# Kernel optimization log

Measured on AMD Instinct MI355X. Metric: run time of the kernel, lower is better.

The kernel has to match this reference:

```python
import jax, jax.numpy as jnp
import numpy as np

N, D_IN, D, E, B = 30000, 512, 512, 300000, 4096
N_RES, N_DNN = 2, 2
EPS = 1e-5


def _ln(x, g, b):
    mu = jnp.mean(x, axis=-1, keepdims=True)
    var = jnp.mean((x - mu) ** 2, axis=-1, keepdims=True)
    return (x - mu) * jax.lax.rsqrt(var + EPS) * g + b


def setup_inputs() -> dict:
    key = jax.random.key(0)
    ks = jax.random.split(key, 16)
    s = 1.0 / np.sqrt(D)
    inp = {
        "node_feat": jax.random.normal(ks[0], (N, D_IN), jnp.float32),
        "edge_hop0": jax.random.randint(ks[1], (2, E), 0, N, jnp.int32),
        "edge_hop1": jax.random.randint(ks[2], (2, E), 0, N, jnp.int32),
        "target_idx": jax.random.randint(ks[3], (B,), 0, N, jnp.int32),
        # node transform
        "Wt": jax.random.normal(ks[4], (D_IN, D), jnp.float32) / np.sqrt(D_IN),
        "bt": jnp.zeros((D,), jnp.float32),
        # GATConv (shared across both hops, one relation)
        "Wf": jax.random.normal(ks[5], (D, D), jnp.float32) * s,
        "bf": jnp.zeros((D,), jnp.float32),
        "w_att": jax.random.normal(ks[6], (2 * D,), jnp.float32) * s,
        "b_att": jnp.zeros((), jnp.float32),
        "gat_bias": jnp.zeros((D,), jnp.float32),
        # Res_DNN
        "Wp": jax.random.normal(ks[7], (D, D), jnp.float32) * s,
        "bp": jnp.zeros((D,), jnp.float32),
        "dnn_W": jax.random.normal(ks[8], (N_RES, N_DNN, D, D), jnp.float32) * s,
        "dnn_b": jnp.zeros((N_RES, N_DNN, D), jnp.float32),
        "dnn_g": jnp.ones((N_RES, N_DNN, D), jnp.float32),
        "dnn_beta": jnp.zeros((N_RES, N_DNN, D), jnp.float32),
        "res_g": jnp.ones((N_RES, D), jnp.float32),
        "res_beta": jnp.zeros((N_RES, D), jnp.float32),
        "Wc": jax.random.normal(ks[9], (D, 1), jnp.float32) * s,
        "bc": jnp.zeros((1,), jnp.float32),
    }
    return inp


def _gat(feat, edges, Wf, bf, w_att, b_att, gat_bias):
    # dst and src are the same node set / same features here
    h = feat @ Wf + bf                      # [N, D]
    di, si = edges[0], edges[1]             # [E], [E]
    # att(concat(dst_h, src_h)) == dst_h @ w[:D] + src_h @ w[D:] + b
    sd = h @ w_att[:D]                      # [N]
    ss = h @ w_att[D:]                      # [N]
    e = jnp.tanh(sd[di] + ss[si] + b_att)   # [E]
    # sparse softmax per destination row
    m = jax.ops.segment_max(e, di, num_segments=N)
    a = jnp.exp(e - m[di])
    denom = jax.ops.segment_sum(a, di, num_segments=N)
    alpha = a / denom[di]                   # [E]
    # sparse-mm aggregation
    out = jax.ops.segment_sum(alpha[:, None] * h[si], di, num_segments=N)
    return out + gat_bias


def reference(node_feat, edge_hop0, edge_hop1, target_idx, Wt, bt, Wf, bf,
              w_att, b_att, gat_bias, Wp, bp, dnn_W, dnn_b, dnn_g, dnn_beta,
              res_g, res_beta, Wc, bc):
    # node-type feature transform (dropout is identity at inference)
    feat = node_feat @ Wt + bt              # [N, D]
    # hops processed from last to first: hop1 then hop0
    for edges in (edge_hop1, edge_hop0):
        g = _gat(feat, edges, Wf, bf, w_att, b_att, gat_bias)
        feat = (feat + g) * 0.5             # mean of stacked [orig, gat_out]
    h = feat[target_idx]                    # [B, D]
    # Res_DNN head
    h = h @ Wp + bp
    for r in range(N_RES):
        sc = h
        for i in range(N_DNN):
            h = _ln(jnp.tanh(h @ dnn_W[r, i] + dnn_b[r, i]), dnn_g[r, i], dnn_beta[r, i])
        h = _ln(jnp.tanh(sc + h), res_g[r], res_beta[r])
    logits = h @ Wc + bc                    # [B, 1]
    return jax.nn.sigmoid(logits)
```

## Files before the change

### kernel.cpp

```cpp
#include <hip/hip_runtime.h>

#define D 512
typedef unsigned short ushort_t;
typedef __attribute__((ext_vector_type(8))) short bf16x8;
typedef __attribute__((ext_vector_type(4))) float f32x4;

static __device__ __forceinline__ ushort_t f2bf(float f) {
  unsigned u = __float_as_uint(f);
  u += 0x7fffu + ((u >> 16) & 1u);
  return (ushort_t)(u >> 16);
}
static __device__ __forceinline__ float bf2f(ushort_t h) {
  return __uint_as_float(((unsigned)h) << 16);
}

static __device__ __forceinline__ void gld_lds16(const void* g, void* lds) {
  __builtin_amdgcn_global_load_lds(
      (const __attribute__((address_space(1))) unsigned int*)g,
      (__attribute__((address_space(3))) unsigned int*)lds, 16, 0, 0);
}

__global__ __launch_bounds__(256) void pack_weight(
    const float* __restrict__ W, ushort_t* __restrict__ out, int K, int N, int nmat) {
  int i = blockIdx.x * 256 + threadIdx.x;
  const int per = K * N;
  if (i >= per * nmat) return;
  const int mat = i / per;
  const int r = i - mat * per;
  const int k = r / N, n = r - k * N;
  const int nt = n >> 4, col = n & 15, kt = k >> 5, kg = (k >> 3) & 3, j = k & 7;
  out[(size_t)mat * per + (((size_t)nt * (K >> 5) + kt) << 9) + ((kg << 4) + col) * 8 + j] =
      f2bf(W[(size_t)mat * per + r]);
}

__global__ __launch_bounds__(256) void conv_bf16_pad(
    const float* __restrict__ in, ushort_t* __restrict__ out, int M, int Mp, int K) {
  const size_t i4 = ((size_t)blockIdx.x * 256 + threadIdx.x) * 4;
  if (i4 >= (size_t)Mp * K) return;
  const int row = (int)(i4 / K);
  ushort4 o;
  if (row < M) {
    const float4 v = *reinterpret_cast<const float4*>(&in[i4]);
    o.x = f2bf(v.x); o.y = f2bf(v.y); o.z = f2bf(v.z); o.w = f2bf(v.w);
  } else {
    o.x = o.y = o.z = o.w = 0;
  }
  *reinterpret_cast<ushort4*>(&out[i4]) = o;
}

__global__ __launch_bounds__(256) void gemm_mfma(
    const ushort_t* __restrict__ A, const ushort_t* __restrict__ Bp,
    const float* __restrict__ bias, ushort_t* __restrict__ C16, int N, int K) {
  __shared__ __align__(16) ushort_t As[2][8 * 512];
  __shared__ __align__(16) ushort_t Bs[2][8 * 512];
  const int nwg = gridDim.x;
  const int q = nwg >> 3, rm = nwg & 7;
  const int xcd = blockIdx.x & 7, kk = blockIdx.x >> 3;
  const int lin = (xcd < rm ? xcd * (q + 1) : rm * (q + 1) + (xcd - rm) * q) + kk;
  const int m0 = (lin >> 2) * 128;
  const int n0 = (lin & 3) * 128;
  const int tid = threadIdx.x;
  const int lane = tid & 63;
  const int wid = tid >> 6;
  const int wm = wid >> 1, wn = wid & 1;
  const int arow = lane & 15;
  const int akoff = (lane >> 4) * 8;
  const int kt32 = K >> 5;
  f32x4 acc[4][4] = {};

  auto stage = [&](int kt, int b) {
    const int k0 = kt * 32;
    gld_lds16(&A[(size_t)(m0 + (wid * 2 + 0) * 16 + arow) * K + k0 + akoff],
              &As[b][(wid * 2 + 0) * 512]);
    gld_lds16(&A[(size_t)(m0 + (wid * 2 + 1) * 16 + arow) * K + k0 + akoff],
              &As[b][(wid * 2 + 1) * 512]);
    gld_lds16(&Bp[(((size_t)(n0 / 16 + wid * 2 + 0) * kt32 + kt) << 9) + lane * 8],
              &Bs[b][(wid * 2 + 0) * 512]);
    gld_lds16(&Bp[(((size_t)(n0 / 16 + wid * 2 + 1) * kt32 + kt) << 9) + lane * 8],
              &Bs[b][(wid * 2 + 1) * 512]);
  };

  stage(0, 0);
  __syncthreads();
  int cur = 0;
  for (int t = 0; t < kt32; ++t) {
    if (t + 1 < kt32) stage(t + 1, cur ^ 1);
    bf16x8 af[4], bfr[4];
#pragma unroll
    for (int mi = 0; mi < 4; ++mi)
      af[mi] = *reinterpret_cast<const bf16x8*>(&As[cur][(wm * 4 + mi) * 512 + lane * 8]);
#pragma unroll
    for (int ni = 0; ni < 4; ++ni)
      bfr[ni] = *reinterpret_cast<const bf16x8*>(&Bs[cur][(wn * 4 + ni) * 512 + lane * 8]);
#pragma unroll
    for (int mi = 0; mi < 4; ++mi)
#pragma unroll
      for (int ni = 0; ni < 4; ++ni)
        acc[mi][ni] = __builtin_amdgcn_mfma_f32_16x16x32_bf16(af[mi], bfr[ni], acc[mi][ni], 0, 0, 0);
    __syncthreads();
    cur ^= 1;
  }
#pragma unroll
  for (int mi = 0; mi < 4; ++mi) {
    const int row = m0 + wm * 64 + mi * 16 + ((lane >> 4) << 2);
#pragma unroll
    for (int ni = 0; ni < 4; ++ni) {
      const int col = n0 + wn * 64 + ni * 16 + (lane & 15);
      const float bv = bias[col];
#pragma unroll
      for (int r = 0; r < 4; ++r)
        C16[(size_t)(row + r) * N + col] = f2bf(acc[mi][ni][r] + bv);
    }
  }
}

__global__ __launch_bounds__(256) void rowdot2_w(
    const ushort_t* __restrict__ hb, const float* __restrict__ w_att,
    float* __restrict__ sd, float* __restrict__ ss, int Nn) {
  const int r = blockIdx.x * 4 + (threadIdx.x >> 6);
  const int lane = threadIdx.x & 63;
  if (r >= Nn) return;
  const bf16x8 hv = *reinterpret_cast<const bf16x8*>(&hb[(size_t)r * D + lane * 8]);
  float d0 = 0.f, d1 = 0.f;
#pragma unroll
  for (int q = 0; q < 8; ++q) {
    const float v = bf2f((ushort_t)hv[q]);
    d0 += v * w_att[lane * 8 + q];
    d1 += v * w_att[D + lane * 8 + q];
  }
#pragma unroll
  for (int off = 32; off > 0; off >>= 1) {
    d0 += __shfl_xor(d0, off);
    d1 += __shfl_xor(d1, off);
  }
  if (lane == 0) { sd[r] = d0; ss[r] = d1; }
}

__global__ void count_deg2(const int* __restrict__ e1, const int* __restrict__ e0,
                           int* __restrict__ deg, int Nn, int E) {
  const int e = blockIdx.x * blockDim.x + threadIdx.x;
  if (e < E) {
    atomicAdd(&deg[e1[e]], 1);
    atomicAdd(&deg[Nn + e0[e]], 1);
  }
}

__global__ __launch_bounds__(256) void scan_block(
    const int* __restrict__ deg, int* __restrict__ incl, int* __restrict__ bsum, int n) {
  __shared__ int buf[256];
  const int t = threadIdx.x;
  const int i = blockIdx.x * 256 + t;
  const int v = (i < n) ? deg[i] : 0;
  buf[t] = v;
  __syncthreads();
  for (int off = 1; off < 256; off <<= 1) {
    const int y = (t >= off) ? buf[t - off] : 0;
    __syncthreads();
    buf[t] += y;
    __syncthreads();
  }
  if (i < n) incl[i] = buf[t];
  if (t == 255) bsum[blockIdx.x] = buf[255];
}

__global__ __launch_bounds__(256) void scan_sums(
    int* __restrict__ bsum, int nb, int* __restrict__ row_total) {
  __shared__ int buf[256];
  const int t = threadIdx.x;
  const int v = (t < nb) ? bsum[t] : 0;
  buf[t] = v;
  __syncthreads();
  for (int off = 1; off < 256; off <<= 1) {
    const int y = (t >= off) ? buf[t - off] : 0;
    __syncthreads();
    buf[t] += y;
    __syncthreads();
  }
  if (t < nb) bsum[t] = buf[t] - v;
  if (t == 0) *row_total = buf[255];
}

__global__ __launch_bounds__(256) void scan_finalize(
    const int* __restrict__ incl, const int* __restrict__ deg,
    const int* __restrict__ bsum, int* __restrict__ row_start,
    int* __restrict__ cursor, int n) {
  const int i = blockIdx.x * 256 + threadIdx.x;
  if (i >= n) return;
  const int v = incl[i] - deg[i] + bsum[i >> 8];
  row_start[i] = v;
  cursor[i] = v;
}

__global__ void fill_csr2(const int* __restrict__ e1, const int* __restrict__ e0,
                          int* __restrict__ cursor, int* __restrict__ csr_s,
                          int Nn, int E) {
  const int e = blockIdx.x * blockDim.x + threadIdx.x;
  if (e >= E) return;
  const int d1 = e1[e];
  csr_s[atomicAdd(&cursor[d1], 1)] = e1[E + e];
  const int d0 = e0[e];
  csr_s[atomicAdd(&cursor[Nn + d0], 1)] = e0[E + e];
}

__global__ __launch_bounds__(256) void gat_aggregate_w(
    ushort_t* __restrict__ featb, const ushort_t* __restrict__ hb,
    const float* __restrict__ sd, const float* __restrict__ ss,
    float* __restrict__ edge_e, const float* __restrict__ b_att_p,
    const float* __restrict__ gat_bias, const int* __restrict__ row_start,
    const int* __restrict__ csr_src, int Nn) {
  const int dst = blockIdx.x * 4 + (threadIdx.x >> 6);
  const int lane = threadIdx.x & 63;
  if (dst >= Nn) return;
  const int beg = row_start[dst];
  const int end = row_start[dst + 1];
  const int deg = end - beg;
  const float sdd = sd[dst];
  const float ba = b_att_p[0];
  const size_t o = (size_t)dst * D + lane * 8;
  bf16x8 fv = *reinterpret_cast<const bf16x8*>(&featb[o]);
  float acc[8] = {};
  if (deg <= 64) {
    const int j0 = beg + lane;
    const bool valid = j0 < end;
    const int slane = valid ? csr_src[j0] : 0;
    const float e = valid ? tanhf(sdd + ss[slane] + ba) : -1e30f;
    float m = e;
#pragma unroll
    for (int off = 32; off > 0; off >>= 1) m = fmaxf(m, __shfl_xor(m, off));
    const float a = valid ? expf(e - m) : 0.f;
    float s = a;
#pragma unroll
    for (int off = 32; off > 0; off >>= 1) s += __shfl_xor(s, off);
    const float w = a * ((s > 0.f) ? 1.f / s : 0.f);
    int k = 0;
    for (; k + 3 < deg; k += 4) {
      const float w0 = __shfl(w, k), w1 = __shfl(w, k + 1);
      const float w2 = __shfl(w, k + 2), w3 = __shfl(w, k + 3);
      const int s0 = __shfl(slane, k), s1 = __shfl(slane, k + 1);
      const int s2 = __shfl(slane, k + 2), s3 = __shfl(slane, k + 3);
      const bf16x8 h0 = *reinterpret_cast<const bf16x8*>(&hb[(size_t)s0 * D + lane * 8]);
      const bf16x8 h1 = *reinterpret_cast<const bf16x8*>(&hb[(size_t)s1 * D + lane * 8]);
      const bf16x8 h2 = *reinterpret_cast<const bf16x8*>(&hb[(size_t)s2 * D + lane * 8]);
      const bf16x8 h3 = *reinterpret_cast<const bf16x8*>(&hb[(size_t)s3 * D + lane * 8]);
#pragma unroll
      for (int qq = 0; qq < 8; ++qq)
        acc[qq] += w0 * bf2f((ushort_t)h0[qq]) + w1 * bf2f((ushort_t)h1[qq]) +
                   w2 * bf2f((ushort_t)h2[qq]) + w3 * bf2f((ushort_t)h3[qq]);
    }
    for (; k < deg; ++k) {
      const float wk = __shfl(w, k);
      const int sk = __shfl(slane, k);
      const bf16x8 h0 = *reinterpret_cast<const bf16x8*>(&hb[(size_t)sk * D + lane * 8]);
#pragma unroll
      for (int qq = 0; qq < 8; ++qq) acc[qq] += wk * bf2f((ushort_t)h0[qq]);
    }
  } else {
    float m = -1e30f;
    for (int j = beg + lane; j < end; j += 64) {
      const float e = tanhf(sdd + ss[csr_src[j]] + ba);
      edge_e[j] = e;
      m = fmaxf(m, e);
    }
#pragma unroll
    for (int off = 32; off > 0; off >>= 1) m = fmaxf(m, __shfl_xor(m, off));
    asm volatile("s_waitcnt vmcnt(0)" ::: "memory");
    float s = 0.f;
    for (int j = beg + lane; j < end; j += 64) {
      const float a2 = expf(edge_e[j] - m);
      edge_e[j] = a2;
      s += a2;
    }
#pragma unroll
    for (int off = 32; off > 0; off >>= 1) s += __shfl_xor(s, off);
    asm volatile("s_waitcnt vmcnt(0)" ::: "memory");
    const float inv = (s > 0.f) ? 1.f / s : 0.f;
    for (int j = beg; j < end; ++j) {
      const float w = edge_e[j] * inv;
      const int sidx = csr_src[j];
      const bf16x8 hv = *reinterpret_cast<const bf16x8*>(&hb[(size_t)sidx * D + lane * 8]);
#pragma unroll
      for (int qq = 0; qq < 8; ++qq) acc[qq] += w * bf2f((ushort_t)hv[qq]);
    }
  }
#pragma unroll
  for (int q = 0; q < 8; ++q) {
    const float f = (bf2f((ushort_t)fv[q]) + acc[q] + gat_bias[lane * 8 + q]) * 0.5f;
    fv[q] = (short)f2bf(f);
  }
  *reinterpret_cast<bf16x8*>(&featb[o]) = fv;
}

__global__ __launch_bounds__(1024, 4) void head_fused(
    const ushort_t* __restrict__ featb, const int* __restrict__ tidx,
    const ushort_t* __restrict__ pWp, const float* __restrict__ bp,
    const ushort_t* __restrict__ pDW, const float* __restrict__ dnn_b,
    const float* __restrict__ dnn_g, const float* __restrict__ dnn_be,
    const float* __restrict__ res_g, const float* __restrict__ res_be,
    const float* __restrict__ Wc, const float* __restrict__ bc,
    float* __restrict__ out) {
  __shared__ __align__(16) ushort_t A_lds[16 * 512];
  __shared__ float lsum[16][16], lsq[16][16], meanv[16], rsv[16];
  const int tid = threadIdx.x;
  const int lane = tid & 63;
  const int wave = tid >> 6;
  const int nt0 = wave * 2;
  const int c15 = lane & 15;
  const int rgrp = lane >> 4;

  {
    const int row = tid >> 6, col8 = tid & 63;
    const int g = tidx[blockIdx.x * 16 + row];
    const bf16x8 v = *reinterpret_cast<const bf16x8*>(&featb[(size_t)g * D + col8 * 8]);
    *reinterpret_cast<bf16x8*>(&A_lds[row * 512 + (col8 ^ (row & 7)) * 8]) = v;
  }
  __syncthreads();

  auto do_gemm = [&](const ushort_t* __restrict__ W, f32x4& a0, f32x4& a1) {
    a0 = f32x4{0.f, 0.f, 0.f, 0.f};
    a1 = f32x4{0.f, 0.f, 0.f, 0.f};
    bf16x8 c0 = *reinterpret_cast<const bf16x8*>(
        &W[(((size_t)nt0 * 16 + 0) << 9) + lane * 8]);
    bf16x8 c1 = *reinterpret_cast<const bf16x8*>(
        &W[(((size_t)(nt0 + 1) * 16 + 0) << 9) + lane * 8]);
#pragma unroll
    for (int kt = 0; kt < 16; ++kt) {
      bf16x8 n0 = c0, n1 = c1;
      if (kt < 15) {
        n0 = *reinterpret_cast<const bf16x8*>(
            &W[(((size_t)nt0 * 16 + kt + 1) << 9) + lane * 8]);
        n1 = *reinterpret_cast<const bf16x8*>(
            &W[(((size_t)(nt0 + 1) * 16 + kt + 1) << 9) + lane * 8]);
      }
      const int col8 = kt * 4 + rgrp;
      const bf16x8 af = *reinterpret_cast<const bf16x8*>(
          &A_lds[c15 * 512 + (col8 ^ (c15 & 7)) * 8]);
      a0 = __builtin_amdgcn_mfma_f32_16x16x32_bf16(af, c0, a0, 0, 0, 0);
      a1 = __builtin_amdgcn_mfma_f32_16x16x32_bf16(af, c1, a1, 0, 0, 0);
      c0 = n0;
      c1 = n1;
    }
  };

  auto block_ln = [&](f32x4& v0, f32x4& v1, const float* __restrict__ g,
                      const float* __restrict__ be) {
    float psum[4], psq[4];
#pragma unroll
    for (int r = 0; r < 4; ++r) {
      psum[r] = v0[r] + v1[r];
      psq[r] = v0[r] * v0[r] + v1[r] * v1[r];
    }
#pragma unroll
    for (int off = 8; off > 0; off >>= 1)
#pragma unroll
      for (int r = 0; r < 4; ++r) {
        psum[r] += __shfl_xor(psum[r], off);
        psq[r] += __shfl_xor(psq[r], off);
      }
    if (c15 == 0) {
#pragma unroll
      for (int r = 0; r < 4; ++r) {
        lsum[wave][rgrp * 4 + r] = psum[r];
        lsq[wave][rgrp * 4 + r] = psq[r];
      }
    }
    __syncthreads();
    if (tid < 16) {
      float s = 0.f, qq = 0.f;
#pragma unroll
      for (int w = 0; w < 16; ++w) { s += lsum[w][tid]; qq += lsq[w][tid]; }
      const float mean = s * (1.f / 512.f);
      const float var = qq * (1.f / 512.f) - mean * mean;
      meanv[tid] = mean;
      rsv[tid] = rsqrtf(var + 1e-5f);
    }
    __syncthreads();
    const int col0 = nt0 * 16 + c15;
    const int col1 = (nt0 + 1) * 16 + c15;
    const float g0 = g[col0], b0 = be[col0];
    const float g1 = g[col1], b1 = be[col1];
#pragma unroll
    for (int r = 0; r < 4; ++r) {
      const int row = rgrp * 4 + r;
      v0[r] = (v0[r] - meanv[row]) * rsv[row] * g0 + b0;
      v1[r] = (v1[r] - meanv[row]) * rsv[row] * g1 + b1;
    }
  };

  auto store_A = [&](const f32x4& v0, const f32x4& v1) {
    const int col0 = nt0 * 16 + c15;
    const int col1 = (nt0 + 1) * 16 + c15;
#pragma unroll
    for (int r = 0; r < 4; ++r) {
      const int row = rgrp * 4 + r;
      A_lds[row * 512 + (((col0 >> 3) ^ (row & 7)) << 3) + (col0 & 7)] = f2bf(v0[r]);
      A_lds[row * 512 + (((col1 >> 3) ^ (row & 7)) << 3) + (col1 & 7)] = f2bf(v1[r]);
    }
  };

  f32x4 sc0, sc1, acc0, acc1, ln0, ln1;

  do_gemm(pWp, acc0, acc1);
  {
    const float bv0 = bp[nt0 * 16 + c15];
    const float bv1 = bp[(nt0 + 1) * 16 + c15];
#pragma unroll
    for (int r = 0; r < 4; ++r) { sc0[r] = acc0[r] + bv0; sc1[r] = acc1[r] + bv1; }
  }
  __syncthreads();
  store_A(sc0, sc1);
  __syncthreads();

  for (int rb = 0; rb < 2; ++rb) {
    {
      const int st = rb * 2;
      do_gemm(pDW + (size_t)st * D * D, acc0, acc1);
      const float bv0 = dnn_b[st * D + nt0 * 16 + c15];
      const float bv1 = dnn_b[st * D + (nt0 + 1) * 16 + c15];
#pragma unroll
      for (int r = 0; r < 4; ++r) {
        acc0[r] = tanhf(acc0[r] + bv0);
        acc1[r] = tanhf(acc1[r] + bv1);
      }
      block_ln(acc0, acc1, dnn_g + st * D, dnn_be + st * D);
      store_A(acc0, acc1);
      __syncthreads();
    }
    {
      const int st = rb * 2 + 1;
      do_gemm(pDW + (size_t)st * D * D, ln0, ln1);
      const float bv0 = dnn_b[st * D + nt0 * 16 + c15];
      const float bv1 = dnn_b[st * D + (nt0 + 1) * 16 + c15];
#pragma unroll
      for (int r = 0; r < 4; ++r) {
        ln0[r] = tanhf(ln0[r] + bv0);
        ln1[r] = tanhf(ln1[r] + bv1);
      }
      block_ln(ln0, ln1, dnn_g + st * D, dnn_be + st * D);
    }
#pragma unroll
    for (int r = 0; r < 4; ++r) {
      acc0[r] = tanhf(sc0[r] + ln0[r]);
      acc1[r] = tanhf(sc1[r] + ln1[r]);
    }
    block_ln(acc0, acc1, res_g + rb * D, res_be + rb * D);
    sc0 = acc0;
    sc1 = acc1;
    if (rb == 0) {
      store_A(sc0, sc1);
      __syncthreads();
    }
  }

  float pr[4];
  {
    const float w0 = Wc[nt0 * 16 + c15];
    const float w1 = Wc[(nt0 + 1) * 16 + c15];
#pragma unroll
    for (int r = 0; r < 4; ++r) pr[r] = sc0[r] * w0 + sc1[r] * w1;
  }
#pragma unroll
  for (int off = 8; off > 0; off >>= 1)
#pragma unroll
    for (int r = 0; r < 4; ++r) pr[r] += __shfl_xor(pr[r], off);
  __syncthreads();
  if (c15 == 0) {
#pragma unroll
    for (int r = 0; r < 4; ++r) lsum[wave][rgrp * 4 + r] = pr[r];
  }
  __syncthreads();
  if (tid < 16) {
    float s = 0.f;
#pragma unroll
    for (int w = 0; w < 16; ++w) s += lsum[w][tid];
    out[blockIdx.x * 16 + tid] = 1.f / (1.f + expf(-(s + bc[0])));
  }
}

extern "C" void kernel_launch(void* const* d_in, const int* in_sizes, int n_in,
                              void* d_out, int out_size, void* d_ws, size_t ws_size,
                              hipStream_t stream) {
  (void)n_in; (void)out_size; (void)ws_size;
  const float* node_feat = (const float*)d_in[0];
  const int* edge0 = (const int*)d_in[1];
  const int* edge1 = (const int*)d_in[2];
  const int* tidx = (const int*)d_in[3];
  const float* Wt = (const float*)d_in[4];
  const float* bt = (const float*)d_in[5];
  const float* Wf = (const float*)d_in[6];
  const float* bfp = (const float*)d_in[7];
  const float* w_att = (const float*)d_in[8];
  const float* b_att = (const float*)d_in[9];
  const float* gat_bias = (const float*)d_in[10];
  const float* Wp = (const float*)d_in[11];
  const float* bp = (const float*)d_in[12];
  const float* dnn_W = (const float*)d_in[13];
  const float* dnn_b = (const float*)d_in[14];
  const float* dnn_g = (const float*)d_in[15];
  const float* dnn_be = (const float*)d_in[16];
  const float* res_g = (const float*)d_in[17];
  const float* res_be = (const float*)d_in[18];
  const float* Wc = (const float*)d_in[19];
  const float* bc = (const float*)d_in[20];
  float* out = (float*)d_out;

  const int Nn = in_sizes[0] / D;
  const int E = in_sizes[1] / 2;
  const int B = in_sizes[3];
  const int K_IN = in_sizes[4] / D;
  const int Mp = (Nn + 127) / 128 * 128;
  const int N2 = 2 * Nn;

  char* p = (char*)d_ws;
  auto alloc = [&](size_t bytes) -> char* {
    char* r = p;
    p += (bytes + 255) & ~(size_t)255;
    return r;
  };
  ushort_t* featb = (ushort_t*)alloc((size_t)Mp * D * 2);
  ushort_t* hb = (ushort_t*)alloc((size_t)Mp * D * 2);
  float* sd = (float*)alloc((size_t)Nn * 4);
  float* ss = (float*)alloc((size_t)Nn * 4);
  int* deg = (int*)alloc((size_t)N2 * 4);
  int* incl = (int*)alloc((size_t)N2 * 4);
  int* bsum = (int*)alloc(256 * 4);
  int* cursor = (int*)alloc((size_t)N2 * 4);
  int* row_start = (int*)alloc((size_t)(N2 + 1) * 4);
  int* csr_s = (int*)alloc((size_t)2 * E * 4);
  float* edge_e = (float*)alloc((size_t)2 * E * 4);
  ushort_t* pWt = (ushort_t*)alloc((size_t)K_IN * D * 2);
  ushort_t* pWf = (ushort_t*)alloc((size_t)D * D * 2);
  ushort_t* pWp = (ushort_t*)alloc((size_t)D * D * 2);
  ushort_t* pDWall = (ushort_t*)alloc((size_t)4 * D * D * 2);

  dim3 blk(256);
  const int nb2 = (N2 + 255) / 256;
  const int nw4 = (Nn + 3) / 4;

  {
    pack_weight<<<(K_IN * D + 255) / 256, blk, 0, stream>>>(Wt, pWt, K_IN, D, 1);
    pack_weight<<<(D * D + 255) / 256, blk, 0, stream>>>(Wf, pWf, D, D, 1);
    pack_weight<<<(D * D + 255) / 256, blk, 0, stream>>>(Wp, pWp, D, D, 1);
    pack_weight<<<(4 * D * D + 255) / 256, blk, 0, stream>>>(dnn_W, pDWall, D, D, 4);
    conv_bf16_pad<<<((size_t)Mp * K_IN / 4 + 255) / 256, blk, 0, stream>>>(
        node_feat, hb , Nn, Mp, K_IN);
  }

  hipMemsetAsync(deg, 0, (size_t)N2 * 4, stream);
  count_deg2<<<(E + 255) / 256, blk, 0, stream>>>(edge1, edge0, deg, Nn, E);
  scan_block<<<nb2, blk, 0, stream>>>(deg, incl, bsum, N2);
  scan_sums<<<1, blk, 0, stream>>>(bsum, nb2, &row_start[N2]);
  scan_finalize<<<nb2, blk, 0, stream>>>(incl, deg, bsum, row_start, cursor, N2);
  fill_csr2<<<(E + 255) / 256, blk, 0, stream>>>(edge1, edge0, cursor, csr_s, Nn, E);

  gemm_mfma<<<dim3(4 * (Mp / 128)), blk, 0, stream>>>(hb, pWt, bt, featb, D, K_IN);

  for (int hp = 0; hp < 2; ++hp) {
    gemm_mfma<<<dim3(4 * (Mp / 128)), blk, 0, stream>>>(featb, pWf, bfp, hb, D, D);
    rowdot2_w<<<nw4, blk, 0, stream>>>(hb, w_att, sd, ss, Nn);
    gat_aggregate_w<<<nw4, blk, 0, stream>>>(featb, hb, sd, ss, edge_e, b_att,
                                             gat_bias, row_start + hp * Nn, csr_s, Nn);
  }

  head_fused<<<B / 16, dim3(1024), 0, stream>>>(
      featb, tidx, pWp, bp, pDWall, dnn_b, dnn_g, dnn_be, res_g, res_be,
      Wc, bc, out);
}
```

Measured before the change: 355.4 us.

## Replace CSR build with fixed-width per-node buckets and edge-scan fallback

Drops the degree count, three-kernel prefix scan and CSR fill. In their place one atomic pass writes each edge's source into a fixed 64-slot bucket per destination node. Nodes with more than 64 incoming edges fall back to scanning the whole edge list, which is slow but correct. The aggregation inner loop is also unrolled from 4 to 8 gathers to keep more loads in flight. This trades several small launches and passes for a larger bucket buffer, and relies on degrees staying at or below 64, which holds for uniform random edges (mean degree about 10).

Measured after the change: 340.7 us. 1.04x faster.

```diff
diff --git a/kernel.cpp b/kernel.cpp
--- a/kernel.cpp
+++ b/kernel.cpp
@@ -136,93 +136,37 @@
   if (lane == 0) { sd[r] = d0; ss[r] = d1; }
 }
 
-__global__ void count_deg2(const int* __restrict__ e1, const int* __restrict__ e0,
-                           int* __restrict__ deg, int Nn, int E) {
-  const int e = blockIdx.x * blockDim.x + threadIdx.x;
-  if (e < E) {
-    atomicAdd(&deg[e1[e]], 1);
-    atomicAdd(&deg[Nn + e0[e]], 1);
-  }
-}
-
-__global__ __launch_bounds__(256) void scan_block(
-    const int* __restrict__ deg, int* __restrict__ incl, int* __restrict__ bsum, int n) {
-  __shared__ int buf[256];
-  const int t = threadIdx.x;
-  const int i = blockIdx.x * 256 + t;
-  const int v = (i < n) ? deg[i] : 0;
-  buf[t] = v;
-  __syncthreads();
-  for (int off = 1; off < 256; off <<= 1) {
-    const int y = (t >= off) ? buf[t - off] : 0;
-    __syncthreads();
-    buf[t] += y;
-    __syncthreads();
-  }
-  if (i < n) incl[i] = buf[t];
-  if (t == 255) bsum[blockIdx.x] = buf[255];
-}
-
-__global__ __launch_bounds__(256) void scan_sums(
-    int* __restrict__ bsum, int nb, int* __restrict__ row_total) {
-  __shared__ int buf[256];
-  const int t = threadIdx.x;
-  const int v = (t < nb) ? bsum[t] : 0;
-  buf[t] = v;
-  __syncthreads();
-  for (int off = 1; off < 256; off <<= 1) {
-    const int y = (t >= off) ? buf[t - off] : 0;
-    __syncthreads();
-    buf[t] += y;
-    __syncthreads();
-  }
-  if (t < nb) bsum[t] = buf[t] - v;
-  if (t == 0) *row_total = buf[255];
-}
-
-__global__ __launch_bounds__(256) void scan_finalize(
-    const int* __restrict__ incl, const int* __restrict__ deg,
-    const int* __restrict__ bsum, int* __restrict__ row_start,
-    int* __restrict__ cursor, int n) {
-  const int i = blockIdx.x * 256 + threadIdx.x;
-  if (i >= n) return;
-  const int v = incl[i] - deg[i] + bsum[i >> 8];
-  row_start[i] = v;
-  cursor[i] = v;
-}
-
-__global__ void fill_csr2(const int* __restrict__ e1, const int* __restrict__ e0,
-                          int* __restrict__ cursor, int* __restrict__ csr_s,
-                          int Nn, int E) {
+__global__ void fill_bucket(const int* __restrict__ e1, const int* __restrict__ e0,
+                            int* __restrict__ cnt, int* __restrict__ bucket,
+                            int Nn, int E) {
   const int e = blockIdx.x * blockDim.x + threadIdx.x;
   if (e >= E) return;
   const int d1 = e1[e];
-  csr_s[atomicAdd(&cursor[d1], 1)] = e1[E + e];
+  const int p1 = atomicAdd(&cnt[d1], 1);
+  if (p1 < 64) bucket[(size_t)d1 * 64 + p1] = e1[E + e];
   const int d0 = e0[e];
-  csr_s[atomicAdd(&cursor[Nn + d0], 1)] = e0[E + e];
+  const int p0 = atomicAdd(&cnt[Nn + d0], 1);
+  if (p0 < 64) bucket[((size_t)(Nn + d0)) * 64 + p0] = e0[E + e];
 }
 
 __global__ __launch_bounds__(256) void gat_aggregate_w(
     ushort_t* __restrict__ featb, const ushort_t* __restrict__ hb,
     const float* __restrict__ sd, const float* __restrict__ ss,
-    float* __restrict__ edge_e, const float* __restrict__ b_att_p,
-    const float* __restrict__ gat_bias, const int* __restrict__ row_start,
-    const int* __restrict__ csr_src, int Nn) {
+    const int* __restrict__ di, const int* __restrict__ si,
+    const float* __restrict__ b_att_p, const float* __restrict__ gat_bias,
+    const int* __restrict__ cnt, const int* __restrict__ bucket, int Nn, int E) {
   const int dst = blockIdx.x * 4 + (threadIdx.x >> 6);
   const int lane = threadIdx.x & 63;
   if (dst >= Nn) return;
-  const int beg = row_start[dst];
-  const int end = row_start[dst + 1];
-  const int deg = end - beg;
+  const int deg = cnt[dst];
   const float sdd = sd[dst];
   const float ba = b_att_p[0];
   const size_t o = (size_t)dst * D + lane * 8;
   bf16x8 fv = *reinterpret_cast<const bf16x8*>(&featb[o]);
   float acc[8] = {};
   if (deg <= 64) {
-    const int j0 = beg + lane;
-    const bool valid = j0 < end;
-    const int slane = valid ? csr_src[j0] : 0;
+    const bool valid = lane < deg;
+    const int slane = valid ? bucket[(size_t)dst * 64 + lane] : 0;
     const float e = valid ? tanhf(sdd + ss[slane] + ba) : -1e30f;
     float m = e;
 #pragma unroll
@@ -233,21 +177,37 @@
     for (int off = 32; off > 0; off >>= 1) s += __shfl_xor(s, off);
     const float w = a * ((s > 0.f) ? 1.f / s : 0.f);
     int k = 0;
-    for (; k + 3 < deg; k += 4) {
+    for (; k + 7 < deg; k += 8) {
+      float wk[8];
+      int sk[8];
+#pragma unroll
+      for (int u = 0; u < 8; ++u) {
+        wk[u] = __shfl(w, k + u);
+        sk[u] = __shfl(slane, k + u);
+      }
+      bf16x8 hv[8];
+#pragma unroll
+      for (int u = 0; u < 8; ++u)
+        hv[u] = *reinterpret_cast<const bf16x8*>(&hb[(size_t)sk[u] * D + lane * 8]);
+#pragma unroll
+      for (int qq = 0; qq < 8; ++qq) {
+        float t0 = wk[0] * bf2f((ushort_t)hv[0][qq]) + wk[1] * bf2f((ushort_t)hv[1][qq]);
+        float t1 = wk[2] * bf2f((ushort_t)hv[2][qq]) + wk[3] * bf2f((ushort_t)hv[3][qq]);
+        float t2 = wk[4] * bf2f((ushort_t)hv[4][qq]) + wk[5] * bf2f((ushort_t)hv[5][qq]);
+        float t3 = wk[6] * bf2f((ushort_t)hv[6][qq]) + wk[7] * bf2f((ushort_t)hv[7][qq]);
+        acc[qq] += (t0 + t1) + (t2 + t3);
+      }
+    }
+    for (; k + 1 < deg; k += 2) {
       const float w0 = __shfl(w, k), w1 = __shfl(w, k + 1);
-      const float w2 = __shfl(w, k + 2), w3 = __shfl(w, k + 3);
       const int s0 = __shfl(slane, k), s1 = __shfl(slane, k + 1);
-      const int s2 = __shfl(slane, k + 2), s3 = __shfl(slane, k + 3);
       const bf16x8 h0 = *reinterpret_cast<const bf16x8*>(&hb[(size_t)s0 * D + lane * 8]);
       const bf16x8 h1 = *reinterpret_cast<const bf16x8*>(&hb[(size_t)s1 * D + lane * 8]);
-      const bf16x8 h2 = *reinterpret_cast<const bf16x8*>(&hb[(size_t)s2 * D + lane * 8]);
-      const bf16x8 h3 = *reinterpret_cast<const bf16x8*>(&hb[(size_t)s3 * D + lane * 8]);
 #pragma unroll
       for (int qq = 0; qq < 8; ++qq)
-        acc[qq] += w0 * bf2f((ushort_t)h0[qq]) + w1 * bf2f((ushort_t)h1[qq]) +
-                   w2 * bf2f((ushort_t)h2[qq]) + w3 * bf2f((ushort_t)h3[qq]);
-    }
-    for (; k < deg; ++k) {
+        acc[qq] += w0 * bf2f((ushort_t)h0[qq]) + w1 * bf2f((ushort_t)h1[qq]);
+    }
+    if (k < deg) {
       const float wk = __shfl(w, k);
       const int sk = __shfl(slane, k);
       const bf16x8 h0 = *reinterpret_cast<const bf16x8*>(&hb[(size_t)sk * D + lane * 8]);
@@ -256,30 +216,31 @@
     }
   } else {
     float m = -1e30f;
-    for (int j = beg + lane; j < end; j += 64) {
-      const float e = tanhf(sdd + ss[csr_src[j]] + ba);
-      edge_e[j] = e;
-      m = fmaxf(m, e);
-    }
+    for (int e = lane; e < E; e += 64)
+      if (di[e] == dst) m = fmaxf(m, tanhf(sdd + ss[si[e]] + ba));
 #pragma unroll
     for (int off = 32; off > 0; off >>= 1) m = fmaxf(m, __shfl_xor(m, off));
-    asm volatile("s_waitcnt vmcnt(0)" ::: "memory");
     float s = 0.f;
-    for (int j = beg + lane; j < end; j += 64) {
-      const float a2 = expf(edge_e[j] - m);
-      edge_e[j] = a2;
-      s += a2;
-    }
+    for (int e = lane; e < E; e += 64)
+      if (di[e] == dst) s += expf(tanhf(sdd + ss[si[e]] + ba) - m);
 #pragma unroll
     for (int off = 32; off > 0; off >>= 1) s += __shfl_xor(s, off);
-    asm volatile("s_waitcnt vmcnt(0)" ::: "memory");
     const float inv = (s > 0.f) ? 1.f / s : 0.f;
-    for (int j = beg; j < end; ++j) {
-      const float w = edge_e[j] * inv;
-      const int sidx = csr_src[j];
-      const bf16x8 hv = *reinterpret_cast<const bf16x8*>(&hb[(size_t)sidx * D + lane * 8]);
-#pragma unroll
-      for (int qq = 0; qq < 8; ++qq) acc[qq] += w * bf2f((ushort_t)hv[qq]);
+    for (int base = 0; base < E; base += 64) {
+      const int e = base + lane;
+      const bool hit = (e < E) && (di[e] == dst);
+      unsigned long long mask = __ballot(hit);
+      const int sidx = hit ? si[e] : 0;
+      const float aval = hit ? expf(tanhf(sdd + ss[sidx] + ba) - m) * inv : 0.f;
+      while (mask) {
+        const int l = __ffsll((long long)mask) - 1;
+        mask &= mask - 1;
+        const float wv = __shfl(aval, l);
+        const int sk = __shfl(sidx, l);
+        const bf16x8 hv = *reinterpret_cast<const bf16x8*>(&hb[(size_t)sk * D + lane * 8]);
+#pragma unroll
+        for (int qq = 0; qq < 8; ++qq) acc[qq] += wv * bf2f((ushort_t)hv[qq]);
+      }
     }
   }
 #pragma unroll
@@ -520,20 +481,14 @@
   ushort_t* hb = (ushort_t*)alloc((size_t)Mp * D * 2);
   float* sd = (float*)alloc((size_t)Nn * 4);
   float* ss = (float*)alloc((size_t)Nn * 4);
-  int* deg = (int*)alloc((size_t)N2 * 4);
-  int* incl = (int*)alloc((size_t)N2 * 4);
-  int* bsum = (int*)alloc(256 * 4);
-  int* cursor = (int*)alloc((size_t)N2 * 4);
-  int* row_start = (int*)alloc((size_t)(N2 + 1) * 4);
-  int* csr_s = (int*)alloc((size_t)2 * E * 4);
-  float* edge_e = (float*)alloc((size_t)2 * E * 4);
+  int* cnt = (int*)alloc((size_t)N2 * 4);
+  int* bucket = (int*)alloc((size_t)N2 * 64 * 4);
   ushort_t* pWt = (ushort_t*)alloc((size_t)K_IN * D * 2);
   ushort_t* pWf = (ushort_t*)alloc((size_t)D * D * 2);
   ushort_t* pWp = (ushort_t*)alloc((size_t)D * D * 2);
   ushort_t* pDWall = (ushort_t*)alloc((size_t)4 * D * D * 2);
 
   dim3 blk(256);
-  const int nb2 = (N2 + 255) / 256;
   const int nw4 = (Nn + 3) / 4;
 
   {
@@ -545,20 +500,18 @@
         node_feat, hb , Nn, Mp, K_IN);
   }
 
-  hipMemsetAsync(deg, 0, (size_t)N2 * 4, stream);
-  count_deg2<<<(E + 255) / 256, blk, 0, stream>>>(edge1, edge0, deg, Nn, E);
-  scan_block<<<nb2, blk, 0, stream>>>(deg, incl, bsum, N2);
-  scan_sums<<<1, blk, 0, stream>>>(bsum, nb2, &row_start[N2]);
-  scan_finalize<<<nb2, blk, 0, stream>>>(incl, deg, bsum, row_start, cursor, N2);
-  fill_csr2<<<(E + 255) / 256, blk, 0, stream>>>(edge1, edge0, cursor, csr_s, Nn, E);
+  hipMemsetAsync(cnt, 0, (size_t)N2 * 4, stream);
+  fill_bucket<<<(E + 255) / 256, blk, 0, stream>>>(edge1, edge0, cnt, bucket, Nn, E);
 
   gemm_mfma<<<dim3(4 * (Mp / 128)), blk, 0, stream>>>(hb, pWt, bt, featb, D, K_IN);
 
+  const int* hops[2] = {edge1, edge0};
   for (int hp = 0; hp < 2; ++hp) {
     gemm_mfma<<<dim3(4 * (Mp / 128)), blk, 0, stream>>>(featb, pWf, bfp, hb, D, D);
     rowdot2_w<<<nw4, blk, 0, stream>>>(hb, w_att, sd, ss, Nn);
-    gat_aggregate_w<<<nw4, blk, 0, stream>>>(featb, hb, sd, ss, edge_e, b_att,
-                                             gat_bias, row_start + hp * Nn, csr_s, Nn);
+    gat_aggregate_w<<<nw4, blk, 0, stream>>>(
+        featb, hb, sd, ss, hops[hp], hops[hp] + E, b_att, gat_bias,
+        cnt + hp * Nn, bucket + (size_t)hp * Nn * 64, Nn, E);
   }
 
   head_fused<<<B / 16, dim3(1024), 0, stream>>>(
```
